# Kernel optimization log

Measured on AMD Instinct MI355X. Metric: run time of the kernel, lower is better.

Reference implementation:

```python
import jax, jax.numpy as jnp
import numpy as np

HEADS = 8  # init heads


def setup_inputs() -> dict:
    key = jax.random.key(0)
    k1, k2, k3, k4 = jax.random.split(key, 4)
    B, C, L = 32, 512, 32  # batch, dim, lateral_size
    x = jax.random.normal(k1, (B, C, L, L), dtype=jnp.float32)
    # 1x1 conv with no bias == per-pixel matmul; store as [3*dim, dim]
    qkv_w = jax.random.normal(k2, (3 * C, C), dtype=jnp.float32) * (1.0 / np.sqrt(C))
    h_pos = jax.random.normal(k3, (L, 1, C), dtype=jnp.float32) * 0.02
    w_pos = jax.random.normal(k4, (1, L, C), dtype=jnp.float32) * 0.02
    return {"x": x, "qkv_w": qkv_w, "h_pos": h_pos, "w_pos": w_pos}


def reference(x, qkv_w, h_pos, w_pos):
    B, C, H, W = x.shape
    p = HEADS
    d = C // p
    n = H * W
    # QKV 1x1 conv -> [B, 3C, H, W]
    qkv = jnp.einsum('oc,bchw->bohw', qkv_w, x)
    q, k, v = jnp.split(qkv, 3, axis=1)
    # 'b (p d) h w -> b p (h w) d'
    def to_heads(t):
        return t.reshape(B, p, d, H, W).transpose(0, 1, 3, 4, 2).reshape(B, p, n, d)
    q, k, v = to_heads(q), to_heads(k), to_heads(v)
    # relative pos: [H,1,C] + [1,W,C] -> [H,W,C]; 'h w (p d) -> p (h w) d'
    rp = (h_pos + w_pos).reshape(H, W, p, d).transpose(2, 0, 1, 3).reshape(p, n, d)
    # content-position + content-content scores: [B, p, n, n]
    scores = jnp.einsum('bpnd,pmd->bpnm', q, rp) + jnp.einsum('bpnd,bpmd->bpnm', q, k)
    attn = jax.nn.softmax(scores, axis=-1)
    out = jnp.einsum('bpnm,bpmd->bpnd', attn, v)
    # 'b p (h w) d -> b (p d) h w'
    return out.reshape(B, p, H, W, d).transpose(0, 1, 4, 2, 3).reshape(B, C, H, W)
```

## Files before the change

kernel.cpp:

```cpp
#include <hip/hip_runtime.h>
#include <hip/hip_bf16.h>
#include <hip/hip_fp16.h>

#define HEADS 8
#define BB 32
#define CC 512
#define NN 1024
#define DD 64

typedef _Float16 f16;
typedef __attribute__((ext_vector_type(8))) _Float16 f16x8;
typedef __attribute__((ext_vector_type(4))) _Float16 f16x4;
typedef __attribute__((ext_vector_type(2))) __fp16 hf16x2;
typedef __attribute__((ext_vector_type(4))) float f32x4;

__device__ __forceinline__ void gload16(const f16* g, f16* l) {
    __builtin_amdgcn_global_load_lds(
        (const __attribute__((address_space(1))) void*)g,
        (__attribute__((address_space(3))) void*)l, 16, 0, 0);
}

__global__ __launch_bounds__(256) void wconv(
    const float* __restrict__ W, f16* __restrict__ Wh)
{
    const size_t i = ((size_t)blockIdx.x * 256 + threadIdx.x) * 8;
    float4 a = *(const float4*)(W + i);
    float4 b = *(const float4*)(W + i + 4);
    f16x8 h = {(f16)a.x, (f16)a.y, (f16)a.z, (f16)a.w,
               (f16)b.x, (f16)b.y, (f16)b.z, (f16)b.w};
    *(f16x8*)(Wh + i) = h;
}

__global__ __launch_bounds__(256) void prep_x(
    const float* __restrict__ x, f16* __restrict__ xt)
{
    __shared__ f16 T[64][65];
    const int tid = threadIdx.x;
    const int c0 = blockIdx.x * 64;
    const int m0 = blockIdx.y * 64;
    const int b  = blockIdx.z;
    const float* xb = x + (size_t)b * CC * NN;

    const int m_l = tid & 63, c_l = tid >> 6;
    #pragma unroll
    for (int s = 0; s < 16; ++s) {
        const int cr = s * 4 + c_l;
        T[cr][m_l] = (f16)xb[(size_t)(c0 + cr) * NN + m0 + m_l];
    }
    __syncthreads();
    const int m_r = tid >> 2, cq = (tid & 3) * 16;
    f16 buf[16];
    #pragma unroll
    for (int j = 0; j < 16; ++j) buf[j] = T[cq + j][m_r];
    f16* dst = xt + ((size_t)b * NN + m0 + m_r) * CC + c0 + cq;
    *(f16x8*)dst       = *(f16x8*)&buf[0];
    *(f16x8*)(dst + 8) = *(f16x8*)&buf[8];
}

__global__ __launch_bounds__(256) void qkv_mfma(
    const f16*  __restrict__ xt,
    const f16*  __restrict__ Wh,
    const float* __restrict__ h_pos,
    const float* __restrict__ w_pos,
    f16* __restrict__ Qh, f16* __restrict__ Kh, f16* __restrict__ Vt)
{
    __shared__ f16 Xs[128 * 64];
    __shared__ f16 Ws[128 * 64];

    const int tid  = threadIdx.x;
    const int wave = tid >> 6, lane = tid & 63;
    const int ln = lane & 15, quad = lane >> 4;

    const unsigned bid  = blockIdx.x;
    const unsigned xcd  = bid & 7;
    const unsigned slot = bid >> 3;
    const unsigned ot   = slot % 12u;
    const unsigned mt   = xcd * 32u + slot / 12u;
    const int o0  = (int)ot * 128;
    const int mg0 = (int)mt * 128;
    const int mw = (wave & 1) * 64, ow = (wave >> 1) * 64;

    f32x4 acc[4][4];
    #pragma unroll
    for (int ia = 0; ia < 4; ++ia)
        #pragma unroll
        for (int ib = 0; ib < 4; ++ib) acc[ia][ib] = (f32x4){0.f, 0.f, 0.f, 0.f};

    const int sr = wave * 32 + (lane >> 3);
    const int sc = (lane & 7) * 8;
    const f16* xg = xt + (size_t)(mg0 + sr) * CC + sc;
    const f16* wg = Wh + (size_t)(o0  + sr) * CC + sc;
    f16* xl = &Xs[(wave * 32) * 64];
    f16* wl = &Ws[(wave * 32) * 64];

    for (int ct = 0; ct < 8; ++ct) {
        const int c0 = ct * 64;
        __syncthreads();
        #pragma unroll
        for (int i = 0; i < 4; ++i) {
            gload16(xg + (size_t)i * 8 * CC + c0, xl + i * 8 * 64);
            gload16(wg + (size_t)i * 8 * CC + c0, wl + i * 8 * 64);
        }
        __syncthreads();
        #pragma unroll
        for (int ks = 0; ks < 2; ++ks) {
            f16x8 a[4], bf[4];
            #pragma unroll
            for (int f = 0; f < 4; ++f) {
                a[f]  = *(const f16x8*)&Xs[(mw + f * 16 + ln) * 64 + ks * 32 + quad * 8];
                bf[f] = *(const f16x8*)&Ws[(ow + f * 16 + ln) * 64 + ks * 32 + quad * 8];
            }
            #pragma unroll
            for (int ia = 0; ia < 4; ++ia)
                #pragma unroll
                for (int ib = 0; ib < 4; ++ib)
                    acc[ia][ib] = __builtin_amdgcn_mfma_f32_16x16x32_f16(
                        a[ia], bf[ib], acc[ia][ib], 0, 0, 0);
        }
    }

    const int region = o0 >> 9;
    const int ob = o0 + ow;
    const int p  = (ob >> 6) & 7;
    const int b  = mg0 >> 10;
    const int n0 = (mg0 & 1023) + mw;

    if (region < 2) {
        f16* dst = (region == 0) ? Qh : Kh;
        const size_t hb = (size_t)(b * HEADS + p) * NN * DD;
        #pragma unroll
        for (int ib = 0; ib < 4; ++ib) {
            const int d = ib * 16 + ln;
            #pragma unroll
            for (int ia = 0; ia < 4; ++ia) {
                #pragma unroll
                for (int r = 0; r < 4; ++r) {
                    const int n = n0 + ia * 16 + quad * 4 + r;
                    float v = acc[ia][ib][r];
                    if (region == 1) {
                        const int c = p * DD + d;
                        v += h_pos[(n >> 5) * CC + c] + w_pos[(n & 31) * CC + c];
                    }
                    dst[hb + (size_t)n * DD + d] = (f16)v;
                }
            }
        }
    } else {
        const size_t vb = (size_t)(b * HEADS + p) * DD * NN;
        #pragma unroll
        for (int ib = 0; ib < 4; ++ib) {
            const int d = ib * 16 + ln;
            #pragma unroll
            for (int ia = 0; ia < 4; ++ia) {
                const int n = n0 + ia * 16 + quad * 4;
                f16x4 pk = {(f16)acc[ia][ib][0], (f16)acc[ia][ib][1],
                            (f16)acc[ia][ib][2], (f16)acc[ia][ib][3]};
                *(f16x4*)&Vt[vb + (size_t)d * NN + n] = pk;
            }
        }
    }
}

#define KST 72

__global__ __launch_bounds__(256) void attn_kernel(
    const f16* __restrict__ Qh, const f16* __restrict__ Kh,
    const f16* __restrict__ Vt, float* __restrict__ out)
{
    __shared__ f16 KS [64 * KST];
    __shared__ f16 VtS[64 * KST];
    __shared__ f16 PS [4][16 * KST];

    const int tid  = threadIdx.x;
    const int wave = tid >> 6;
    const int lane = tid & 63;
    const int ln   = lane & 15;
    const int quad = lane >> 4;

    const unsigned bid  = blockIdx.x;
    const unsigned xcd  = bid & 7;
    const unsigned slot = bid >> 3;
    const int qt = (int)(slot & 15u);
    const unsigned g = xcd * 32u + (slot >> 4);
    const int b = (int)(g >> 3);
    const int p = (int)(g & 7u);
    const size_t hb = (size_t)(b * HEADS + p) * NN * DD;

    const int qrow = qt * 64 + wave * 16 + ln;
    f16x8 qf[2];
    #pragma unroll
    for (int ks = 0; ks < 2; ++ks)
        qf[ks] = *(const f16x8*)(Qh + hb + (size_t)qrow * DD + ks * 32 + quad * 8);

    f32x4 o[4];
    #pragma unroll
    for (int dt = 0; dt < 4; ++dt) o[dt] = (f32x4){0.f, 0.f, 0.f, 0.f};
    float lrun = 0.f;
    float mrun = -__builtin_inff();

    const int sr = tid >> 2, sc = (tid & 3) * 16;

    f16x8 kreg0, kreg1, vreg0, vreg1;
    {
        const size_t gk = hb + (size_t)sr * DD + sc;
        kreg0 = *(const f16x8*)(Kh + gk);
        kreg1 = *(const f16x8*)(Kh + gk + 8);
        const size_t gv = hb + (size_t)sr * NN + sc;
        vreg0 = *(const f16x8*)(Vt + gv);
        vreg1 = *(const f16x8*)(Vt + gv + 8);
    }

    f16* Pw = &PS[wave][0];

    for (int kt = 0; kt < 16; ++kt) {
        __syncthreads();
        *(f16x8*)&KS [sr * KST + sc]     = kreg0;
        *(f16x8*)&KS [sr * KST + sc + 8] = kreg1;
        *(f16x8*)&VtS[sr * KST + sc]     = vreg0;
        *(f16x8*)&VtS[sr * KST + sc + 8] = vreg1;
        if (kt < 15) {
            const size_t gk = hb + (size_t)((kt + 1) * 64 + sr) * DD + sc;
            kreg0 = *(const f16x8*)(Kh + gk);
            kreg1 = *(const f16x8*)(Kh + gk + 8);
            const size_t gv = hb + (size_t)sr * NN + (kt + 1) * 64 + sc;
            vreg0 = *(const f16x8*)(Vt + gv);
            vreg1 = *(const f16x8*)(Vt + gv + 8);
        }
        __syncthreads();

        f32x4 s[4];
        #pragma unroll
        for (int nt = 0; nt < 4; ++nt) s[nt] = (f32x4){0.f, 0.f, 0.f, 0.f};
        #pragma unroll
        for (int ks = 0; ks < 2; ++ks) {
            #pragma unroll
            for (int nt = 0; nt < 4; ++nt) {
                f16x8 bk = *(const f16x8*)&KS[(nt * 16 + ln) * KST + ks * 32 + quad * 8];
                s[nt] = __builtin_amdgcn_mfma_f32_16x16x32_f16(bk, qf[ks], s[nt], 0, 0, 0);
            }
        }

        float mx = s[0][0];
        #pragma unroll
        for (int nt = 0; nt < 4; ++nt)
            #pragma unroll
            for (int r = 0; r < 4; ++r) mx = fmaxf(mx, s[nt][r]);
        mx = fmaxf(mx, __shfl_xor(mx, 16));
        mx = fmaxf(mx, __shfl_xor(mx, 32));
        const float mnew = fmaxf(mrun, mx);
        const float alpha = __expf(mrun - mnew);
        mrun = mnew;

        float lsum = 0.f;
        #pragma unroll
        for (int nt = 0; nt < 4; ++nt) {
            const float p0 = __expf(s[nt][0] - mrun);
            const float p1 = __expf(s[nt][1] - mrun);
            const float p2 = __expf(s[nt][2] - mrun);
            const float p3 = __expf(s[nt][3] - mrun);
            lsum += (p0 + p1) + (p2 + p3);
            hf16x2 lo = __builtin_amdgcn_cvt_pkrtz(p0, p1);
            hf16x2 hi = __builtin_amdgcn_cvt_pkrtz(p2, p3);
            f16x4 pk = {(f16)lo.x, (f16)lo.y, (f16)hi.x, (f16)hi.y};
            *(f16x4*)&Pw[ln * KST + nt * 16 + quad * 4] = pk;
        }
        lsum += __shfl_xor(lsum, 16);
        lsum += __shfl_xor(lsum, 32);
        lrun = lrun * alpha + lsum;

        #pragma unroll
        for (int dt = 0; dt < 4; ++dt) {
            o[dt][0] *= alpha; o[dt][1] *= alpha;
            o[dt][2] *= alpha; o[dt][3] *= alpha;
        }

        asm volatile("s_waitcnt lgkmcnt(0)" ::: "memory");

        #pragma unroll
        for (int ks = 0; ks < 2; ++ks) {
            f16x8 pa = *(const f16x8*)&Pw[ln * KST + ks * 32 + quad * 8];
            #pragma unroll
            for (int dt = 0; dt < 4; ++dt) {
                f16x8 vb = *(const f16x8*)&VtS[(dt * 16 + ln) * KST + ks * 32 + quad * 8];
                o[dt] = __builtin_amdgcn_mfma_f32_16x16x32_f16(vb, pa, o[dt], 0, 0, 0);
            }
        }
    }

    const float inv = 1.0f / lrun;
    const int nq = qt * 64 + wave * 16 + ln;
    #pragma unroll
    for (int dt = 0; dt < 4; ++dt) {
        const int c = p * DD + dt * 16 + quad * 4;
        #pragma unroll
        for (int r = 0; r < 4; ++r)
            out[((size_t)b * CC + c + r) * NN + nq] = o[dt][r] * inv;
    }
}

extern "C" void kernel_launch(void* const* d_in, const int* in_sizes, int n_in,
                              void* d_out, int out_size, void* d_ws, size_t ws_size,
                              hipStream_t stream) {
    const float* x     = (const float*)d_in[0];
    const float* qkv_w = (const float*)d_in[1];
    const float* h_pos = (const float*)d_in[2];
    const float* w_pos = (const float*)d_in[3];
    float* out = (float*)d_out;

    const size_t PT = (size_t)BB * HEADS * NN * DD;
    f16* xt = (f16*)d_ws;
    f16* Qh = xt + PT;
    f16* Kh = Qh + PT;
    f16* Vt = Kh + PT;
    f16* Wh = Vt + PT;

    wconv<<<dim3(3 * CC * CC / (256 * 8)), 256, 0, stream>>>(qkv_w, Wh);
    prep_x<<<dim3(CC / 64, NN / 64, BB), 256, 0, stream>>>(x, xt);
    qkv_mfma<<<dim3(3072), 256, 0, stream>>>(xt, Wh, h_pos, w_pos, Qh, Kh, Vt);
    attn_kernel<<<dim3(4096), 256, 0, stream>>>(Qh, Kh, Vt, out);
}
```

Measured before the change: 381.2 us.

## Stage QKV epilogue through LDS for coalesced stores; lazy softmax rescale with exp2

The QKV GEMM epilogue now writes each wave's accumulator tile into shared memory and then emits coalesced 16-byte global stores for Q, K and the transposed V, replacing scattered 2-byte and 8-byte writes. Q is pre-scaled by log2(e) so the attention kernel can use the native exp2 instruction instead of expf. The online softmax only rescales the running max, sum and output when some row's max exceeds the current max by a threshold, skipping the alpha multiplies on most iterations. The threshold bounds unnormalised exponentials to roughly 2^11.5, which fits in fp16 but trades some headroom against overflow, and the reused shared buffer needs an extra barrier.

```diff
diff --git a/kernel.cpp b/kernel.cpp
--- a/kernel.cpp
+++ b/kernel.cpp
@@ -18,6 +18,10 @@
     __builtin_amdgcn_global_load_lds(
         (const __attribute__((address_space(1))) void*)g,
         (__attribute__((address_space(3))) void*)l, 16, 0, 0);
+}
+
+__device__ __forceinline__ void wavefence() {
+    asm volatile("s_waitcnt lgkmcnt(0)" ::: "memory");
 }
 
 __global__ __launch_bounds__(256) void wconv(
@@ -64,8 +68,9 @@
     const float* __restrict__ w_pos,
     f16* __restrict__ Qh, f16* __restrict__ Kh, f16* __restrict__ Vt)
 {
-    __shared__ f16 Xs[128 * 64];
-    __shared__ f16 Ws[128 * 64];
+    __shared__ f16 SM[2 * 128 * 64];
+    f16* Xs = SM;
+    f16* Ws = SM + 128 * 64;
 
     const int tid  = threadIdx.x;
     const int wave = tid >> 6, lane = tid & 63;
@@ -119,6 +124,9 @@
         }
     }
 
+    __syncthreads();
+    f16* Ep = SM + wave * 4096;
+
     const int region = o0 >> 9;
     const int ob = o0 + ow;
     const int p  = (ob >> 6) & 7;
@@ -129,34 +137,64 @@
         f16* dst = (region == 0) ? Qh : Kh;
         const size_t hb = (size_t)(b * HEADS + p) * NN * DD;
         #pragma unroll
-        for (int ib = 0; ib < 4; ++ib) {
-            const int d = ib * 16 + ln;
-            #pragma unroll
-            for (int ia = 0; ia < 4; ++ia) {
+        for (int ph = 0; ph < 2; ++ph) {
+            #pragma unroll
+            for (int ibl = 0; ibl < 2; ++ibl) {
+                const int ib = ph * 2 + ibl;
+                const int d  = ib * 16 + ln;
+                const int dl = ibl * 16 + ln;
                 #pragma unroll
-                for (int r = 0; r < 4; ++r) {
-                    const int n = n0 + ia * 16 + quad * 4 + r;
-                    float v = acc[ia][ib][r];
-                    if (region == 1) {
-                        const int c = p * DD + d;
-                        v += h_pos[(n >> 5) * CC + c] + w_pos[(n & 31) * CC + c];
+                for (int ia = 0; ia < 4; ++ia) {
+                    #pragma unroll
+                    for (int r = 0; r < 4; ++r) {
+                        const int nl = ia * 16 + quad * 4 + r;
+                        float v = acc[ia][ib][r];
+                        if (region == 0) {
+                            v *= 1.44269504f;
+                        } else {
+                            const int n = n0 + nl;
+                            const int c = p * DD + d;
+                            v += h_pos[(n >> 5) * CC + c] + w_pos[(n & 31) * CC + c];
+                        }
+                        Ep[nl * 34 + dl] = (f16)v;
                     }
-                    dst[hb + (size_t)n * DD + d] = (f16)v;
                 }
             }
+            wavefence();
+            #pragma unroll
+            for (int j = 0; j < 4; ++j) {
+                const int nl = (lane >> 2) + 16 * j;
+                const int dc = (lane & 3) * 8;
+                f16x8 row = *(const f16x8*)&Ep[nl * 34 + dc];
+                *(f16x8*)(dst + hb + (size_t)(n0 + nl) * DD + ph * 32 + dc) = row;
+            }
+            wavefence();
         }
     } else {
         const size_t vb = (size_t)(b * HEADS + p) * DD * NN;
         #pragma unroll
-        for (int ib = 0; ib < 4; ++ib) {
-            const int d = ib * 16 + ln;
-            #pragma unroll
-            for (int ia = 0; ia < 4; ++ia) {
-                const int n = n0 + ia * 16 + quad * 4;
-                f16x4 pk = {(f16)acc[ia][ib][0], (f16)acc[ia][ib][1],
-                            (f16)acc[ia][ib][2], (f16)acc[ia][ib][3]};
-                *(f16x4*)&Vt[vb + (size_t)d * NN + n] = pk;
-            }
+        for (int ph = 0; ph < 2; ++ph) {
+            #pragma unroll
+            for (int ibl = 0; ibl < 2; ++ibl) {
+                const int ib = ph * 2 + ibl;
+                const int dl = ibl * 16 + ln;
+                #pragma unroll
+                for (int ia = 0; ia < 4; ++ia) {
+                    const int nl = ia * 16 + quad * 4;
+                    f16x4 pk = {(f16)acc[ia][ib][0], (f16)acc[ia][ib][1],
+                                (f16)acc[ia][ib][2], (f16)acc[ia][ib][3]};
+                    *(f16x4*)&Ep[dl * 68 + nl] = pk;
+                }
+            }
+            wavefence();
+            #pragma unroll
+            for (int j = 0; j < 4; ++j) {
+                const int dl = (lane >> 3) + 8 * j;
+                const int nc = (lane & 7) * 8;
+                f16x8 row = *(const f16x8*)&Ep[dl * 68 + nc];
+                *(f16x8*)(Vt + vb + (size_t)(ph * 32 + dl) * NN + n0 + nc) = row;
+            }
+            wavefence();
         }
     }
 }
@@ -197,6 +235,7 @@
     for (int dt = 0; dt < 4; ++dt) o[dt] = (f32x4){0.f, 0.f, 0.f, 0.f};
     float lrun = 0.f;
     float mrun = -__builtin_inff();
+    const float THR = 11.5416f;
 
     const int sr = tid >> 2, sc = (tid & 3) * 16;
 
@@ -247,17 +286,26 @@
             for (int r = 0; r < 4; ++r) mx = fmaxf(mx, s[nt][r]);
         mx = fmaxf(mx, __shfl_xor(mx, 16));
         mx = fmaxf(mx, __shfl_xor(mx, 32));
-        const float mnew = fmaxf(mrun, mx);
-        const float alpha = __expf(mrun - mnew);
-        mrun = mnew;
+
+        if (__any(mx > mrun + THR)) {
+            const float mnew = fmaxf(mrun, mx);
+            const float alpha = __builtin_amdgcn_exp2f(mrun - mnew);
+            mrun = mnew;
+            lrun *= alpha;
+            #pragma unroll
+            for (int dt = 0; dt < 4; ++dt) {
+                o[dt][0] *= alpha; o[dt][1] *= alpha;
+                o[dt][2] *= alpha; o[dt][3] *= alpha;
+            }
+        }
 
         float lsum = 0.f;
         #pragma unroll
         for (int nt = 0; nt < 4; ++nt) {
-            const float p0 = __expf(s[nt][0] - mrun);
-            const float p1 = __expf(s[nt][1] - mrun);
-            const float p2 = __expf(s[nt][2] - mrun);
-            const float p3 = __expf(s[nt][3] - mrun);
+            const float p0 = __builtin_amdgcn_exp2f(s[nt][0] - mrun);
+            const float p1 = __builtin_amdgcn_exp2f(s[nt][1] - mrun);
+            const float p2 = __builtin_amdgcn_exp2f(s[nt][2] - mrun);
+            const float p3 = __builtin_amdgcn_exp2f(s[nt][3] - mrun);
             lsum += (p0 + p1) + (p2 + p3);
             hf16x2 lo = __builtin_amdgcn_cvt_pkrtz(p0, p1);
             hf16x2 hi = __builtin_amdgcn_cvt_pkrtz(p2, p3);
@@ -266,13 +314,7 @@
         }
         lsum += __shfl_xor(lsum, 16);
         lsum += __shfl_xor(lsum, 32);
-        lrun = lrun * alpha + lsum;
-
-        #pragma unroll
-        for (int dt = 0; dt < 4; ++dt) {
-            o[dt][0] *= alpha; o[dt][1] *= alpha;
-            o[dt][2] *= alpha; o[dt][3] *= alpha;
-        }
+        lrun += lsum;
 
         asm volatile("s_waitcnt lgkmcnt(0)" ::: "memory");
 
```

Result: faster. 368.7 us (-3.3%).
